# Optimization experiments

Measured on AMD Instinct MI355X. Metric: run time of the kernel, lower is better.

Reference implementation:

```python
import jax, jax.numpy as jnp
import numpy as np

EPS = 1e-6

def setup_inputs() -> dict:
    key = jax.random.key(0)
    ks = jax.random.split(key, 5)
    B, NH, S, DH = 2, 4, 2048, 128
    return {
        "q": jax.random.normal(ks[0], (B, NH, S, DH), dtype=jnp.float32),
        "k": jax.random.normal(ks[1], (B, NH, S, DH), dtype=jnp.float32),
        "v": jax.random.normal(ks[2], (B, NH, S, DH), dtype=jnp.float32),
        "i": jax.random.normal(ks[3], (B, NH, S), dtype=jnp.float32),
        "f": jax.random.normal(ks[4], (B, NH, S), dtype=jnp.float32),
    }

def _mlstm(q, k, v, i, f):
    # q,k,v: [B,NH,S,DH]; i,f: [B,NH,S] gate pre-activations.
    B, NH, S, DH = q.shape
    q = q * (DH ** -0.5)
    f_log = jax.nn.log_sigmoid(f)  # log forget gate

    # time-major for scan: [S, B, NH, ...]
    qT = jnp.moveaxis(q, 2, 0)
    kT = jnp.moveaxis(k, 2, 0)
    vT = jnp.moveaxis(v, 2, 0)
    iT = jnp.moveaxis(i, 2, 0)
    fT = jnp.moveaxis(f_log, 2, 0)

    C0 = jnp.zeros((B, NH, DH, DH), dtype=q.dtype)  # matrix memory C
    n0 = jnp.zeros((B, NH, DH), dtype=q.dtype)      # normalizer state n
    m0 = jnp.zeros((B, NH), dtype=q.dtype)          # max-stabilizer state m

    def step(carry, xs):
        C, n, m = carry
        q_t, k_t, v_t, i_t, fl_t = xs
        m_new = jnp.maximum(fl_t + m, i_t)               # [B,NH]
        a = jnp.exp(fl_t + m - m_new)                    # decay scale
        b = jnp.exp(i_t - m_new)                         # input scale
        C_new = a[..., None, None] * C + b[..., None, None] * (
            k_t[..., :, None] * v_t[..., None, :])       # [B,NH,DH,DH]
        n_new = a[..., None] * n + b[..., None] * k_t    # [B,NH,DH]
        h_num = jnp.einsum('bhd,bhde->bhe', q_t, C_new)  # [B,NH,DH]
        qn = jnp.einsum('bhd,bhd->bh', q_t, n_new)
        denom = jnp.maximum(jnp.abs(qn), jnp.exp(-m_new)) + EPS
        h = h_num / denom[..., None]
        return (C_new, n_new, m_new), h

    _, hT = jax.lax.scan(step, (C0, n0, m0), (qT, kT, vT, iT, fT))
    return jnp.moveaxis(hT, 0, 2)  # [B,NH,S,DH]

def reference(q, k, v, i, f):
    return _mlstm(q, k, v, i, f)
```

## Files before the change

kernel.cpp:

```cpp
#include <hip/hip_runtime.h>
#include <math.h>


typedef _Float16 f16;
typedef _Float16 f16x4 __attribute__((ext_vector_type(4)));
typedef _Float16 f16x8 __attribute__((ext_vector_type(8)));
typedef float    f32x4 __attribute__((ext_vector_type(4)));

#define S_LEN  2048
#define DHD    128
#define NHEADS 8
#define QT     32
#define KT     128
#define EPS    1e-6f

#define KH_OFF  0
#define KL_OFF  32768
#define VTH_OFF 65536
#define VTL_OFF 98304
#define BS_OFF  131072
#define QNL_OFF 131712
#define SMEM_BYTES 132224
#define PART_OFF 0

__device__ __forceinline__ int kswz(int row, int byteInRow) {
  return row * 256 + (byteInRow ^ ((row & 15) << 4));
}
__device__ __forceinline__ int vswz(int e, int byteInRow) {
  return e * 256 + (byteInRow ^ ((e & 15) << 4) ^ (((e >> 4) & 1) << 3));
}

__device__ __forceinline__ f32x4 mfma16(f16x8 a, f16x8 b, f32x4 c) {
  return __builtin_amdgcn_mfma_f32_16x16x32_f16(a, b, c, 0, 0, 0);
}

__global__ __launch_bounds__(256) void mlstm_scan(
    const float* __restrict__ ig_all, const float* __restrict__ fg_all,
    float* __restrict__ bf, float* __restrict__ Mf, float* __restrict__ en)
{
  const int hd  = blockIdx.x;
  const int tid = threadIdx.x;
  __shared__ double sc[256];
  const float* fg = fg_all + (size_t)hd * S_LEN;
  const float* ig = ig_all + (size_t)hd * S_LEN;
  const int base = tid * 8;

  double v[8];
#pragma unroll
  for (int u = 0; u < 8; ++u) {
    float x = fg[base + u];
    float fl = fminf(x, 0.0f) - log1pf(expf(-fabsf(x)));
    v[u] = (double)fl;
  }
#pragma unroll
  for (int u = 1; u < 8; ++u) v[u] += v[u - 1];
  sc[tid] = v[7];
  __syncthreads();
  for (int off = 1; off < 256; off <<= 1) {
    double t = (tid >= off) ? sc[tid - off] : 0.0;
    __syncthreads();
    sc[tid] += t;
    __syncthreads();
  }
  const double excl = sc[tid] - v[7];

  double F[8], b[8];
#pragma unroll
  for (int u = 0; u < 8; ++u) {
    F[u] = v[u] + excl;
    b[u] = (double)ig[base + u] - F[u];
    bf[(size_t)hd * S_LEN + base + u] = (float)b[u];
  }
  __syncthreads();
  double mv[8];
  mv[0] = b[0];
#pragma unroll
  for (int u = 1; u < 8; ++u) mv[u] = fmax(mv[u - 1], b[u]);
  sc[tid] = mv[7];
  __syncthreads();
  for (int off = 1; off < 256; off <<= 1) {
    double t = (tid >= off) ? sc[tid - off] : -1.0e300;
    __syncthreads();
    sc[tid] = fmax(sc[tid], t);
    __syncthreads();
  }
  const double exclm = (tid > 0) ? sc[tid - 1] : -1.0e300;
  double run = exclm;
#pragma unroll
  for (int u = 0; u < 8; ++u) {
    run = fmax(run, b[u]);
    double Mt = fmax(0.0, run);
    Mf[(size_t)hd * S_LEN + base + u] = (float)Mt;
    en[(size_t)hd * S_LEN + base + u] = (float)exp(-(F[u] + Mt));
  }
}

__global__ __launch_bounds__(256, 1) void mlstm_main(
    const float* __restrict__ qg, const float* __restrict__ kg, const float* __restrict__ vg,
    const float* __restrict__ bf, const float* __restrict__ Mf, const float* __restrict__ en,
    float* __restrict__ outg)
{
  extern __shared__ char smem[];
  const int bid  = blockIdx.x;
  const int hd   = bid & 7;
  const int qt32 = 63 - (bid >> 3);
  const int t0   = qt32 * QT;
  const int tid  = threadIdx.x;
  const int w    = tid >> 6;
  const int lane = tid & 63;
  const int c    = lane & 15;
  const int g    = lane >> 4;

  const size_t hbase = (size_t)hd * S_LEN;
  const float* qg_h = qg + (hbase + t0) * DHD;
  const float* kg_h = kg + hbase * DHD;
  const float* vg_h = vg + hbase * DHD;
  float* bs_lds = (float*)(smem + BS_OFF);

  constexpr float QSC = 0.08838834764831845f;
  f16x8 qfh[2][4], qfl[2][4];
#pragma unroll
  for (int qt = 0; qt < 2; ++qt) {
    const float* qrow = qg_h + (size_t)(16 * qt + c) * DHD;
#pragma unroll
    for (int kc = 0; kc < 4; ++kc) {
      const float* p = qrow + kc * 32 + 8 * g;
      float4 a = *(const float4*)p;
      float4 b = *(const float4*)(p + 4);
      float xs[8] = {a.x, a.y, a.z, a.w, b.x, b.y, b.z, b.w};
#pragma unroll
      for (int s = 0; s < 8; ++s) {
        float x = xs[s] * QSC;
        f16 hi = (f16)x;
        qfh[qt][kc][s] = hi;
        qfl[qt][kc][s] = (f16)(x - (float)hi);
      }
    }
  }

  float Mq[2];
  Mq[0] = Mf[hbase + t0 + c];
  Mq[1] = Mf[hbase + t0 + 16 + c];

  const f32x4 z4 = {0.f, 0.f, 0.f, 0.f};
  f32x4 hacc[2][8];
#pragma unroll
  for (int qt = 0; qt < 2; ++qt)
#pragma unroll
    for (int et = 0; et < 8; ++et) hacc[qt][et] = z4;
  float qn[2] = {0.f, 0.f};

  const int n_iters = qt32 / 4 + 1;
  for (int it = 0; it < n_iters; ++it) {
    const int s0 = it * KT;
    __syncthreads();

    {
      const int colq = tid & 31;
      const int r0 = tid >> 5;
#pragma unroll
      for (int pass = 0; pass < 16; ++pass) {
        const int row = pass * 8 + r0;
        float4 kv4 = *(const float4*)(kg_h + (size_t)(s0 + row) * DHD + colq * 4);
        float xs[4] = {kv4.x, kv4.y, kv4.z, kv4.w};
        f16x4 hi, lo;
#pragma unroll
        for (int s = 0; s < 4; ++s) { f16 h = (f16)xs[s]; hi[s] = h; lo[s] = (f16)(xs[s] - (float)h); }
        const int byte = kswz(row, colq * 8);
        *(f16x4*)(smem + KH_OFF + byte) = hi;
        *(f16x4*)(smem + KL_OFF + byte) = lo;
      }
      const int e   = tid & 127;
      const int kq0 = tid >> 7;
#pragma unroll
      for (int pass = 0; pass < 16; ++pass) {
        const int kvq = pass * 2 + kq0;
        const int kvb = kvq * 4;
        float xs[4];
#pragma unroll
        for (int r = 0; r < 4; ++r) xs[r] = vg_h[(size_t)(s0 + kvb + r) * DHD + e];
        f16x4 hi, lo;
#pragma unroll
        for (int s = 0; s < 4; ++s) { f16 h = (f16)xs[s]; hi[s] = h; lo[s] = (f16)(xs[s] - (float)h); }
        const int byte = vswz(e, kvq * 8);
        *(f16x4*)(smem + VTH_OFF + byte) = hi;
        *(f16x4*)(smem + VTL_OFF + byte) = lo;
      }
      if (tid < 128) bs_lds[tid] = bf[hbase + s0 + tid];
    }
    __syncthreads();

    f32x4 sacc[2][2];
    sacc[0][0] = z4; sacc[0][1] = z4; sacc[1][0] = z4; sacc[1][1] = z4;
    const int kvrow = 32 * w + c;
#pragma unroll
    for (int kc = 0; kc < 4; ++kc) {
      const int cb = kc * 64 + 16 * g;
      f16x8 kh0 = *(const f16x8*)(smem + KH_OFF + kswz(kvrow,      cb));
      f16x8 kl0 = *(const f16x8*)(smem + KL_OFF + kswz(kvrow,      cb));
      f16x8 kh1 = *(const f16x8*)(smem + KH_OFF + kswz(kvrow + 16, cb));
      f16x8 kl1 = *(const f16x8*)(smem + KL_OFF + kswz(kvrow + 16, cb));
#pragma unroll
      for (int qt = 0; qt < 2; ++qt) {
        sacc[qt][0] = mfma16(kh0, qfh[qt][kc], sacc[qt][0]);
        sacc[qt][0] = mfma16(kh0, qfl[qt][kc], sacc[qt][0]);
        sacc[qt][0] = mfma16(kl0, qfh[qt][kc], sacc[qt][0]);
        sacc[qt][1] = mfma16(kh1, qfh[qt][kc], sacc[qt][1]);
        sacc[qt][1] = mfma16(kh1, qfl[qt][kc], sacc[qt][1]);
        sacc[qt][1] = mfma16(kl1, qfh[qt][kc], sacc[qt][1]);
      }
    }

    f32x4 b0 = *(const f32x4*)(bs_lds + 32 * w + 4 * g);
    f32x4 b1 = *(const f32x4*)(bs_lds + 32 * w + 16 + 4 * g);
    f16x8 pfh[2], pfl[2];
#pragma unroll
    for (int qt = 0; qt < 2; ++qt) {
      const int qglob = t0 + 16 * qt + c;
#pragma unroll
      for (int r = 0; r < 4; ++r) {
        const int kv0 = s0 + 32 * w + 4 * g + r;
        const int kv1 = kv0 + 16;
        float p0 = (kv0 <= qglob) ? __expf(b0[r] - Mq[qt]) * sacc[qt][0][r] : 0.f;
        float p1 = (kv1 <= qglob) ? __expf(b1[r] - Mq[qt]) * sacc[qt][1][r] : 0.f;
        qn[qt] += p0 + p1;
        f16 h0 = (f16)p0; pfh[qt][r]     = h0; pfl[qt][r]     = (f16)(p0 - (float)h0);
        f16 h1 = (f16)p1; pfh[qt][r + 4] = h1; pfl[qt][r + 4] = (f16)(p1 - (float)h1);
      }
    }

#pragma unroll
    for (int et = 0; et < 8; ++et) {
      const int e = 16 * et + c;
      const int b0b = (32 * w + 4 * g) * 2;
      const int b1b = (32 * w + 16 + 4 * g) * 2;
      f16x4 vh0 = *(const f16x4*)(smem + VTH_OFF + vswz(e, b0b));
      f16x4 vh1 = *(const f16x4*)(smem + VTH_OFF + vswz(e, b1b));
      f16x4 vl0 = *(const f16x4*)(smem + VTL_OFF + vswz(e, b0b));
      f16x4 vl1 = *(const f16x4*)(smem + VTL_OFF + vswz(e, b1b));
      f16x8 vfh, vfl;
#pragma unroll
      for (int s = 0; s < 4; ++s) {
        vfh[s] = vh0[s]; vfh[s + 4] = vh1[s];
        vfl[s] = vl0[s]; vfl[s + 4] = vl1[s];
      }
#pragma unroll
      for (int qt = 0; qt < 2; ++qt) {
        hacc[qt][et] = mfma16(pfh[qt], vfh, hacc[qt][et]);
        hacc[qt][et] = mfma16(pfh[qt], vfl, hacc[qt][et]);
        hacc[qt][et] = mfma16(pfl[qt], vfh, hacc[qt][et]);
      }
    }
  }

#pragma unroll
  for (int qt = 0; qt < 2; ++qt) {
    qn[qt] += __shfl_xor(qn[qt], 16);
    qn[qt] += __shfl_xor(qn[qt], 32);
  }
  __syncthreads();
  float* qnl  = (float*)(smem + QNL_OFF);
  float* part = (float*)(smem + PART_OFF);
  if (lane < 16) { qnl[w * 32 + lane] = qn[0]; qnl[w * 32 + 16 + lane] = qn[1]; }
#pragma unroll
  for (int qt = 0; qt < 2; ++qt)
#pragma unroll
    for (int et = 0; et < 8; ++et)
#pragma unroll
      for (int r = 0; r < 4; ++r)
        part[(w * 32 + 16 * qt + 4 * g + r) * 132 + 16 * et + c] = hacc[qt][et][r];
  __syncthreads();

  const int e4 = (tid & 31) * 4;
#pragma unroll
  for (int pass = 0; pass < 4; ++pass) {
    const int q = pass * 8 + (tid >> 5);
    f32x4 s = {0.f, 0.f, 0.f, 0.f};
#pragma unroll
    for (int wv = 0; wv < 4; ++wv) {
      const float* pp = part + (wv * 32 + q) * 132 + e4;
      s[0] += pp[0]; s[1] += pp[1]; s[2] += pp[2]; s[3] += pp[3];
    }
    const float qns = qnl[q] + qnl[32 + q] + qnl[64 + q] + qnl[96 + q];
    const float den = fmaxf(fabsf(qns), en[hbase + t0 + q]) + EPS;
    const float inv = 1.0f / den;
    float4 o = make_float4(s[0] * inv, s[1] * inv, s[2] * inv, s[3] * inv);
    *(float4*)(outg + (hbase + t0 + q) * DHD + e4) = o;
  }
}

extern "C" void kernel_launch(void* const* d_in, const int* in_sizes, int n_in,
                              void* d_out, int out_size, void* d_ws, size_t ws_size,
                              hipStream_t stream) {
  (void)in_sizes; (void)n_in; (void)out_size; (void)ws_size;
  const float* q  = (const float*)d_in[0];
  const float* k  = (const float*)d_in[1];
  const float* v  = (const float*)d_in[2];
  const float* ii = (const float*)d_in[3];
  const float* ff = (const float*)d_in[4];
  float* out = (float*)d_out;

  float* bf = (float*)d_ws;
  float* Mf = bf + NHEADS * S_LEN;
  float* en = Mf + NHEADS * S_LEN;

  hipFuncSetAttribute(reinterpret_cast<const void*>(mlstm_main),
                      hipFuncAttributeMaxDynamicSharedMemorySize, SMEM_BYTES);
  mlstm_scan<<<dim3(NHEADS), dim3(256), 0, stream>>>(ii, ff, bf, Mf, en);
  mlstm_main<<<dim3(512), dim3(256), SMEM_BYTES, stream>>>(q, k, v, bf, Mf, en, out);
}
```

Before: 166.3 us.

## Precompute fp16 hi/lo K/V panels and stream them into LDS asynchronously

Adds prep kernels that split K and transposed V into swizzled fp16 hi/lo panels in workspace once per call. The main kernel then copies these panels directly into LDS with global_load_lds instead of converting them per tile. It also shrinks the KV tile to 64, splits the work across waves as 2 query halves by 2 KV halves, and halves LDS use so two blocks fit per CU. Blocks are interleaved so heavy and light causal tiles alternate. The cost is two extra launches, the extra workspace traffic, and a fallback path kept for when the workspace is too small.

```diff
diff --git a/kernel.cpp b/kernel.cpp
--- a/kernel.cpp
+++ b/kernel.cpp
@@ -10,28 +10,28 @@
 #define S_LEN  2048
 #define DHD    128
 #define NHEADS 8
-#define QT     32
-#define KT     128
 #define EPS    1e-6f
 
-#define KH_OFF  0
-#define KL_OFF  32768
-#define VTH_OFF 65536
-#define VTL_OFF 98304
-#define BS_OFF  131072
-#define QNL_OFF 131712
-#define SMEM_BYTES 132224
-#define PART_OFF 0
+#define KHI_F 0
+#define KLO_F 16384
+#define VHI_F 32768
+#define VLO_F 49152
+#define BS_F  65536
+#define QNL_F 65792
+#define SMEM_FAST 66048
 
 __device__ __forceinline__ int kswz(int row, int byteInRow) {
   return row * 256 + (byteInRow ^ ((row & 15) << 4));
 }
-__device__ __forceinline__ int vswz(int e, int byteInRow) {
-  return e * 256 + (byteInRow ^ ((e & 15) << 4) ^ (((e >> 4) & 1) << 3));
-}
-
+__device__ __forceinline__ int vswz64(int e, int byteInRow) {
+  return e * 128 + (byteInRow ^ ((e & 15) << 3));
+}
 __device__ __forceinline__ f32x4 mfma16(f16x8 a, f16x8 b, f32x4 c) {
   return __builtin_amdgcn_mfma_f32_16x16x32_f16(a, b, c, 0, 0, 0);
+}
+__device__ __forceinline__ void gload16(const void* g, void* l) {
+  __builtin_amdgcn_global_load_lds((const __attribute__((address_space(1))) unsigned int*)g,
+                                   (__attribute__((address_space(3))) unsigned int*)l, 16, 0, 0);
 }
 
 __global__ __launch_bounds__(256) void mlstm_scan(
@@ -95,7 +95,239 @@
   }
 }
 
-__global__ __launch_bounds__(256, 1) void mlstm_main(
+__global__ __launch_bounds__(256) void prep_k(
+    const float* __restrict__ kg, char* __restrict__ gkh, char* __restrict__ gkl)
+{
+  const int gid  = blockIdx.x * 256 + threadIdx.x;
+  const int row  = gid >> 2;
+  const int part = gid & 3;
+  const float* src = kg + (size_t)row * DHD;
+  char* oh = gkh + (size_t)row * 256;
+  char* ol = gkl + (size_t)row * 256;
+#pragma unroll
+  for (int j = 0; j < 8; ++j) {
+    float4 x = *(const float4*)(src + j * 16 + part * 4);
+    float xs[4] = {x.x, x.y, x.z, x.w};
+    f16x4 hi, lo;
+#pragma unroll
+    for (int s = 0; s < 4; ++s) { f16 h = (f16)xs[s]; hi[s] = h; lo[s] = (f16)(xs[s] - (float)h); }
+    const int byte = (j * 32 + part * 8) ^ ((row & 15) << 4);
+    *(f16x4*)(oh + byte) = hi;
+    *(f16x4*)(ol + byte) = lo;
+  }
+}
+
+__global__ __launch_bounds__(256) void prep_vt(
+    const float* __restrict__ vg, char* __restrict__ gvh, char* __restrict__ gvl)
+{
+  __shared__ float vts[64][132];
+  const int bid = blockIdx.x;
+  const int head = bid >> 5;
+  const int it   = bid & 31;
+  const int tid  = threadIdx.x;
+
+  {
+    const int r   = tid >> 2;
+    const int seg = tid & 3;
+    const float* src = vg + ((size_t)(head * S_LEN + it * 64 + r)) * DHD;
+#pragma unroll
+    for (int j = 0; j < 8; ++j) {
+      const int c4 = j * 16 + seg * 4;
+      *(float4*)&vts[r][c4] = *(const float4*)(src + c4);
+    }
+  }
+  __syncthreads();
+
+  const int e = tid >> 1;
+  const int h = tid & 1;
+  const size_t tb = (size_t)(head * 32 + it) * 16384 + (size_t)e * 128;
+#pragma unroll
+  for (int i4 = 0; i4 < 8; ++i4) {
+    f16x4 hi, lo;
+#pragma unroll
+    for (int s = 0; s < 4; ++s) {
+      float x = vts[32 * h + i4 * 4 + s][e];
+      f16 hh = (f16)x; hi[s] = hh; lo[s] = (f16)(x - (float)hh);
+    }
+    const int byte = ((32 * h + i4 * 4) * 2) ^ ((e & 15) << 3);
+    *(f16x4*)(gvh + tb + byte) = hi;
+    *(f16x4*)(gvl + tb + byte) = lo;
+  }
+}
+
+__global__ __launch_bounds__(256, 2) void mlstm_fast(
+    const float* __restrict__ qg,
+    const char* __restrict__ gkh, const char* __restrict__ gkl,
+    const char* __restrict__ gvh, const char* __restrict__ gvl,
+    const float* __restrict__ bf, const float* __restrict__ Mf,
+    const float* __restrict__ en, float* __restrict__ outg)
+{
+  extern __shared__ char smem[];
+  const int bid  = blockIdx.x;
+  const int hd   = bid & 7;
+  const int idx  = bid >> 3;
+  const int qt32 = (idx < 32) ? (63 - 2 * idx) : (2 * (idx - 32));
+  const int t0   = qt32 * 32;
+  const int tid  = threadIdx.x;
+  const int w    = tid >> 6;
+  const int lane = tid & 63;
+  const int c    = lane & 15;
+  const int g    = lane >> 4;
+  const int wk   = w & 1;
+  const int qh   = w >> 1;
+
+  const size_t hbase = (size_t)hd * S_LEN;
+  float* bs_lds = (float*)(smem + BS_F);
+
+  constexpr float QSC = 0.08838834764831845f;
+  f16x8 qfh[4], qfl[4];
+  {
+    const float* qrow = qg + (hbase + t0 + 16 * qh + c) * DHD;
+#pragma unroll
+    for (int kc = 0; kc < 4; ++kc) {
+      const float* p = qrow + kc * 32 + 8 * g;
+      float4 a = *(const float4*)p;
+      float4 b = *(const float4*)(p + 4);
+      float xs[8] = {a.x, a.y, a.z, a.w, b.x, b.y, b.z, b.w};
+#pragma unroll
+      for (int s = 0; s < 8; ++s) {
+        float x = xs[s] * QSC;
+        f16 hi = (f16)x;
+        qfh[kc][s] = hi;
+        qfl[kc][s] = (f16)(x - (float)hi);
+      }
+    }
+  }
+  const float Mq = Mf[hbase + t0 + 16 * qh + c];
+
+  const f32x4 z4 = {0.f, 0.f, 0.f, 0.f};
+  f32x4 hacc[8];
+#pragma unroll
+  for (int et = 0; et < 8; ++et) hacc[et] = z4;
+  float qn = 0.f;
+
+  const char* pkh = gkh + hbase * 256;
+  const char* pkl = gkl + hbase * 256;
+  const char* pvh = gvh + (size_t)hd * 524288;
+  const char* pvl = gvl + (size_t)hd * 524288;
+
+  const int n_iters = qt32 / 2 + 1;
+  for (int it = 0; it < n_iters; ++it) {
+    const int s0 = it * 64;
+    __syncthreads();
+
+    {
+      const size_t tb = (size_t)it * 16384;
+#pragma unroll
+      for (int u = 0; u < 4; ++u) {
+        const int off = (w << 12) + (u << 10);
+        const int gl  = off + lane * 16;
+        gload16(pkh + tb + gl, smem + KHI_F + off);
+        gload16(pkl + tb + gl, smem + KLO_F + off);
+        gload16(pvh + tb + gl, smem + VHI_F + off);
+        gload16(pvl + tb + gl, smem + VLO_F + off);
+      }
+      if (tid < 64) bs_lds[tid] = bf[hbase + s0 + tid];
+    }
+    __syncthreads();
+
+    f32x4 sacc0 = z4, sacc1 = z4;
+    const int rowA = 32 * wk + c;
+#pragma unroll
+    for (int kc = 0; kc < 4; ++kc) {
+      const int cb = kc * 64 + 16 * g;
+      f16x8 kh0 = *(const f16x8*)(smem + KHI_F + kswz(rowA,      cb));
+      f16x8 kl0 = *(const f16x8*)(smem + KLO_F + kswz(rowA,      cb));
+      f16x8 kh1 = *(const f16x8*)(smem + KHI_F + kswz(rowA + 16, cb));
+      f16x8 kl1 = *(const f16x8*)(smem + KLO_F + kswz(rowA + 16, cb));
+      sacc0 = mfma16(kh0, qfh[kc], sacc0);
+      sacc0 = mfma16(kh0, qfl[kc], sacc0);
+      sacc0 = mfma16(kl0, qfh[kc], sacc0);
+      sacc1 = mfma16(kh1, qfh[kc], sacc1);
+      sacc1 = mfma16(kh1, qfl[kc], sacc1);
+      sacc1 = mfma16(kl1, qfh[kc], sacc1);
+    }
+
+    f32x4 b0 = *(const f32x4*)(bs_lds + 32 * wk + 4 * g);
+    f32x4 b1 = *(const f32x4*)(bs_lds + 32 * wk + 16 + 4 * g);
+    const int qglob = t0 + 16 * qh + c;
+    f16x8 pfh, pfl;
+#pragma unroll
+    for (int r = 0; r < 4; ++r) {
+      const int kv0 = s0 + 32 * wk + 4 * g + r;
+      const int kv1 = kv0 + 16;
+      float p0 = (kv0 <= qglob) ? __expf(b0[r] - Mq) * sacc0[r] : 0.f;
+      float p1 = (kv1 <= qglob) ? __expf(b1[r] - Mq) * sacc1[r] : 0.f;
+      qn += p0 + p1;
+      f16 h0 = (f16)p0; pfh[r]     = h0; pfl[r]     = (f16)(p0 - (float)h0);
+      f16 h1 = (f16)p1; pfh[r + 4] = h1; pfl[r + 4] = (f16)(p1 - (float)h1);
+    }
+
+    const int byte0 = (64 * wk + 8 * g)      ^ (c << 3);
+    const int byte1 = (64 * wk + 32 + 8 * g) ^ (c << 3);
+#pragma unroll
+    for (int et = 0; et < 8; ++et) {
+      const int eb = (16 * et + c) * 128;
+      f16x4 vh0 = *(const f16x4*)(smem + VHI_F + eb + byte0);
+      f16x4 vh1 = *(const f16x4*)(smem + VHI_F + eb + byte1);
+      f16x4 vl0 = *(const f16x4*)(smem + VLO_F + eb + byte0);
+      f16x4 vl1 = *(const f16x4*)(smem + VLO_F + eb + byte1);
+      f16x8 vfh, vfl;
+#pragma unroll
+      for (int s = 0; s < 4; ++s) {
+        vfh[s] = vh0[s]; vfh[s + 4] = vh1[s];
+        vfl[s] = vl0[s]; vfl[s + 4] = vl1[s];
+      }
+      hacc[et] = mfma16(pfh, vfh, hacc[et]);
+      hacc[et] = mfma16(pfh, vfl, hacc[et]);
+      hacc[et] = mfma16(pfl, vfh, hacc[et]);
+    }
+  }
+
+  qn += __shfl_xor(qn, 16);
+  qn += __shfl_xor(qn, 32);
+  __syncthreads();
+  float* qnl  = (float*)(smem + QNL_F);
+  float* part = (float*)smem;
+  if (lane < 16) qnl[(wk * 2 + qh) * 16 + lane] = qn;
+#pragma unroll
+  for (int et = 0; et < 8; ++et)
+#pragma unroll
+    for (int r = 0; r < 4; ++r)
+      part[(wk * 32 + 16 * qh + 4 * g + r) * 132 + 16 * et + c] = hacc[et][r];
+  __syncthreads();
+
+  const int e4 = (tid & 31) * 4;
+#pragma unroll
+  for (int pass = 0; pass < 4; ++pass) {
+    const int q = pass * 8 + (tid >> 5);
+    const float* pa = part + q * 132 + e4;
+    const float* pb = part + (32 + q) * 132 + e4;
+    f32x4 s;
+#pragma unroll
+    for (int s_ = 0; s_ < 4; ++s_) s[s_] = pa[s_] + pb[s_];
+    const int qhh = q >> 4;
+    const float qns = qnl[qhh * 16 + (q & 15)] + qnl[(2 + qhh) * 16 + (q & 15)];
+    const float den = fmaxf(fabsf(qns), en[hbase + t0 + q]) + EPS;
+    const float inv = 1.0f / den;
+    float4 o = make_float4(s[0] * inv, s[1] * inv, s[2] * inv, s[3] * inv);
+    *(float4*)(outg + (hbase + t0 + q) * DHD + e4) = o;
+  }
+}
+
+#define KH_OFF  0
+#define KL_OFF  32768
+#define VTH_OFF 65536
+#define VTL_OFF 98304
+#define BS_OFF  131072
+#define QNL_OFF 131712
+#define SMEM_FB 132224
+
+__device__ __forceinline__ int vswzfb(int e, int byteInRow) {
+  return e * 256 + (byteInRow ^ ((e & 15) << 4) ^ (((e >> 4) & 1) << 3));
+}
+
+__global__ __launch_bounds__(256, 1) void mlstm_main_fb(
     const float* __restrict__ qg, const float* __restrict__ kg, const float* __restrict__ vg,
     const float* __restrict__ bf, const float* __restrict__ Mf, const float* __restrict__ en,
     float* __restrict__ outg)
@@ -104,7 +336,7 @@
   const int bid  = blockIdx.x;
   const int hd   = bid & 7;
   const int qt32 = 63 - (bid >> 3);
-  const int t0   = qt32 * QT;
+  const int t0   = qt32 * 32;
   const int tid  = threadIdx.x;
   const int w    = tid >> 6;
   const int lane = tid & 63;
@@ -137,7 +369,6 @@
       }
     }
   }
-
   float Mq[2];
   Mq[0] = Mf[hbase + t0 + c];
   Mq[1] = Mf[hbase + t0 + 16 + c];
@@ -152,9 +383,8 @@
 
   const int n_iters = qt32 / 4 + 1;
   for (int it = 0; it < n_iters; ++it) {
-    const int s0 = it * KT;
-    __syncthreads();
-
+    const int s0 = it * 128;
+    __syncthreads();
     {
       const int colq = tid & 31;
       const int r0 = tid >> 5;
@@ -182,7 +412,7 @@
         f16x4 hi, lo;
 #pragma unroll
         for (int s = 0; s < 4; ++s) { f16 h = (f16)xs[s]; hi[s] = h; lo[s] = (f16)(xs[s] - (float)h); }
-        const int byte = vswz(e, kvq * 8);
+        const int byte = vswzfb(e, kvq * 8);
         *(f16x4*)(smem + VTH_OFF + byte) = hi;
         *(f16x4*)(smem + VTL_OFF + byte) = lo;
       }
@@ -234,10 +464,10 @@
       const int e = 16 * et + c;
       const int b0b = (32 * w + 4 * g) * 2;
       const int b1b = (32 * w + 16 + 4 * g) * 2;
-      f16x4 vh0 = *(const f16x4*)(smem + VTH_OFF + vswz(e, b0b));
-      f16x4 vh1 = *(const f16x4*)(smem + VTH_OFF + vswz(e, b1b));
-      f16x4 vl0 = *(const f16x4*)(smem + VTL_OFF + vswz(e, b0b));
-      f16x4 vl1 = *(const f16x4*)(smem + VTL_OFF + vswz(e, b1b));
+      f16x4 vh0 = *(const f16x4*)(smem + VTH_OFF + vswzfb(e, b0b));
+      f16x4 vh1 = *(const f16x4*)(smem + VTH_OFF + vswzfb(e, b1b));
+      f16x4 vl0 = *(const f16x4*)(smem + VTL_OFF + vswzfb(e, b0b));
+      f16x4 vl1 = *(const f16x4*)(smem + VTL_OFF + vswzfb(e, b1b));
       f16x8 vfh, vfl;
 #pragma unroll
       for (int s = 0; s < 4; ++s) {
@@ -260,7 +490,7 @@
   }
   __syncthreads();
   float* qnl  = (float*)(smem + QNL_OFF);
-  float* part = (float*)(smem + PART_OFF);
+  float* part = (float*)smem;
   if (lane < 16) { qnl[w * 32 + lane] = qn[0]; qnl[w * 32 + 16 + lane] = qn[1]; }
 #pragma unroll
   for (int qt = 0; qt < 2; ++qt)
@@ -292,7 +522,7 @@
 extern "C" void kernel_launch(void* const* d_in, const int* in_sizes, int n_in,
                               void* d_out, int out_size, void* d_ws, size_t ws_size,
                               hipStream_t stream) {
-  (void)in_sizes; (void)n_in; (void)out_size; (void)ws_size;
+  (void)in_sizes; (void)n_in; (void)out_size;
   const float* q  = (const float*)d_in[0];
   const float* k  = (const float*)d_in[1];
   const float* v  = (const float*)d_in[2];
@@ -304,8 +534,26 @@
   float* Mf = bf + NHEADS * S_LEN;
   float* en = Mf + NHEADS * S_LEN;
 
-  hipFuncSetAttribute(reinterpret_cast<const void*>(mlstm_main),
-                      hipFuncAttributeMaxDynamicSharedMemorySize, SMEM_BYTES);
+  const size_t PANEL = 4u * 1024 * 1024;
+  const size_t need  = 3u * NHEADS * S_LEN * 4 + 4 * PANEL;
+
   mlstm_scan<<<dim3(NHEADS), dim3(256), 0, stream>>>(ii, ff, bf, Mf, en);
-  mlstm_main<<<dim3(512), dim3(256), SMEM_BYTES, stream>>>(q, k, v, bf, Mf, en, out);
-}
+
+  if (ws_size >= need) {
+    char* gkh = (char*)(en + NHEADS * S_LEN);
+    char* gkl = gkh + PANEL;
+    char* gvh = gkl + PANEL;
+    char* gvl = gvh + PANEL;
+    hipFuncSetAttribute(reinterpret_cast<const void*>(mlstm_fast),
+                        hipFuncAttributeMaxDynamicSharedMemorySize, SMEM_FAST);
+    prep_k <<<dim3(256), dim3(256), 0, stream>>>(k, gkh, gkl);
+    prep_vt<<<dim3(256), dim3(256), 0, stream>>>(v, gvh, gvl);
+    mlstm_fast<<<dim3(512), dim3(256), SMEM_FAST, stream>>>(
+        q, gkh, gkl, gvh, gvl, bf, Mf, en, out);
+  } else {
+    hipFuncSetAttribute(reinterpret_cast<const void*>(mlstm_main_fb),
+                        hipFuncAttributeMaxDynamicSharedMemorySize, SMEM_FB);
+    mlstm_main_fb<<<dim3(512), dim3(256), SMEM_FB, stream>>>(
+        q, k, v, bf, Mf, en, out);
+  }
+}
```

Result: faster. 159.8 us (-3.9%).

## Precompute fp16 hi/lo K/V panels and double-buffer async LDS loads

Applied to the files above, without the earlier changes.

A new prep kernel converts K and V once into swizzled fp16 hi/lo panels in workspace, with V transposed per 64-row tile. The main kernel then streams those panels into LDS with global_load_lds into a double buffer, prefetching the next tile while computing the current one. It also uses 64-query blocks with 64-key tiles split across wave pairs, halving the grid. The aim is to remove the repeated per-block fp32-to-fp16 split and V transpose and to overlap loads with MFMA work. The cost is an extra kernel launch, extra workspace traffic, and fewer blocks, with a heavier causal load imbalance that is no longer reversed-order scheduled.

```diff
diff --git a/kernel.cpp b/kernel.cpp
--- a/kernel.cpp
+++ b/kernel.cpp
@@ -10,28 +10,21 @@
 #define S_LEN  2048
 #define DHD    128
 #define NHEADS 8
-#define QT     32
-#define KT     128
 #define EPS    1e-6f
 
-#define KH_OFF  0
-#define KL_OFF  32768
-#define VTH_OFF 65536
-#define VTL_OFF 98304
-#define BS_OFF  131072
-#define QNL_OFF 131712
-#define SMEM_BYTES 132224
-#define PART_OFF 0
+#define BUFSZ   65536
+#define QNL_OFF 131072
+#define SMEM_BYTES 131584
 
 __device__ __forceinline__ int kswz(int row, int byteInRow) {
   return row * 256 + (byteInRow ^ ((row & 15) << 4));
 }
-__device__ __forceinline__ int vswz(int e, int byteInRow) {
-  return e * 256 + (byteInRow ^ ((e & 15) << 4) ^ (((e >> 4) & 1) << 3));
-}
-
 __device__ __forceinline__ f32x4 mfma16(f16x8 a, f16x8 b, f32x4 c) {
   return __builtin_amdgcn_mfma_f32_16x16x32_f16(a, b, c, 0, 0, 0);
+}
+__device__ __forceinline__ void gload16(const void* g, void* l) {
+  __builtin_amdgcn_global_load_lds((const __attribute__((address_space(1))) unsigned int*)g,
+                                   (__attribute__((address_space(3))) unsigned int*)l, 16, 0, 0);
 }
 
 __global__ __launch_bounds__(256) void mlstm_scan(
@@ -95,33 +88,112 @@
   }
 }
 
-__global__ __launch_bounds__(256, 1) void mlstm_main(
-    const float* __restrict__ qg, const float* __restrict__ kg, const float* __restrict__ vg,
-    const float* __restrict__ bf, const float* __restrict__ Mf, const float* __restrict__ en,
-    float* __restrict__ outg)
+__global__ __launch_bounds__(256) void mlstm_prep(
+    const float* __restrict__ kg, const float* __restrict__ vg,
+    char* __restrict__ gkh, char* __restrict__ gkl,
+    char* __restrict__ gvh, char* __restrict__ gvl)
+{
+  __shared__ float vts[64][132];
+  const int bid = blockIdx.x;
+  const int tid = threadIdx.x;
+
+  if (bid < 256) {
+    const int gid  = bid * 256 + tid;
+    const int row  = gid >> 2;
+    const int part = gid & 3;
+    const float* src = kg + (size_t)row * DHD;
+    char* oh = gkh + (size_t)row * 256;
+    char* ol = gkl + (size_t)row * 256;
+#pragma unroll
+    for (int j = 0; j < 8; ++j) {
+      float4 x = *(const float4*)(src + j * 16 + part * 4);
+      float xs[4] = {x.x, x.y, x.z, x.w};
+      f16x4 hi, lo;
+#pragma unroll
+      for (int s = 0; s < 4; ++s) { f16 h = (f16)xs[s]; hi[s] = h; lo[s] = (f16)(xs[s] - (float)h); }
+      const int byte = (j * 32 + part * 8) ^ ((row & 15) << 4);
+      *(f16x4*)(oh + byte) = hi;
+      *(f16x4*)(ol + byte) = lo;
+    }
+  } else {
+    const int b2   = bid - 256;
+    const int head = b2 >> 5;
+    const int it   = b2 & 31;
+    {
+      const int r   = tid >> 2;
+      const int seg = tid & 3;
+      const float* src = vg + ((size_t)(head * S_LEN + it * 64 + r)) * DHD;
+#pragma unroll
+      for (int j = 0; j < 8; ++j) {
+        const int c4 = j * 16 + seg * 4;
+        *(float4*)&vts[r][c4] = *(const float4*)(src + c4);
+      }
+    }
+    __syncthreads();
+    const int e = tid >> 1;
+    const int h = tid & 1;
+    const size_t tb = (size_t)(head * 32 + it) * 16384 + (size_t)e * 128;
+#pragma unroll
+    for (int i4 = 0; i4 < 8; ++i4) {
+      f16x4 hi, lo;
+#pragma unroll
+      for (int s = 0; s < 4; ++s) {
+        float x = vts[32 * h + i4 * 4 + s][e];
+        f16 hh = (f16)x; hi[s] = hh; lo[s] = (f16)(x - (float)hh);
+      }
+      const int byte = ((32 * h + i4 * 4) * 2) ^ ((e & 15) << 3);
+      *(f16x4*)(gvh + tb + byte) = hi;
+      *(f16x4*)(gvl + tb + byte) = lo;
+    }
+  }
+}
+
+__global__ __launch_bounds__(256, 1) void mlstm_fast2(
+    const float* __restrict__ qg,
+    const char* __restrict__ gkh, const char* __restrict__ gkl,
+    const char* __restrict__ gvh, const char* __restrict__ gvl,
+    const float* __restrict__ bf, const float* __restrict__ Mf,
+    const float* __restrict__ en, float* __restrict__ outg)
 {
   extern __shared__ char smem[];
   const int bid  = blockIdx.x;
   const int hd   = bid & 7;
-  const int qt32 = 63 - (bid >> 3);
-  const int t0   = qt32 * QT;
+  const int j    = bid >> 3;
+  const int t0   = j * 64;
   const int tid  = threadIdx.x;
   const int w    = tid >> 6;
   const int lane = tid & 63;
   const int c    = lane & 15;
   const int g    = lane >> 4;
+  const int wk   = w & 1;
+  const int qp   = w >> 1;
 
   const size_t hbase = (size_t)hd * S_LEN;
-  const float* qg_h = qg + (hbase + t0) * DHD;
-  const float* kg_h = kg + hbase * DHD;
-  const float* vg_h = vg + hbase * DHD;
-  float* bs_lds = (float*)(smem + BS_OFF);
+  const char* pkh = gkh + hbase * 256;
+  const char* pkl = gkl + hbase * 256;
+  const char* pvh = gvh + (size_t)hd * 524288;
+  const char* pvl = gvl + (size_t)hd * 524288;
+
+  const int n_it = j + 1;
+
+  {
+    const size_t tb = 0;
+#pragma unroll
+    for (int u = 0; u < 4; ++u) {
+      const int off = (w << 12) + (u << 10);
+      const int gl  = off + lane * 16;
+      gload16(pkh + tb + gl, smem + 0     + off);
+      gload16(pkl + tb + gl, smem + 16384 + off);
+      gload16(pvh + tb + gl, smem + 32768 + off);
+      gload16(pvl + tb + gl, smem + 49152 + off);
+    }
+  }
 
   constexpr float QSC = 0.08838834764831845f;
   f16x8 qfh[2][4], qfl[2][4];
 #pragma unroll
-  for (int qt = 0; qt < 2; ++qt) {
-    const float* qrow = qg_h + (size_t)(16 * qt + c) * DHD;
+  for (int u = 0; u < 2; ++u) {
+    const float* qrow = qg + (hbase + t0 + 16 * (2 * qp + u) + c) * DHD;
 #pragma unroll
     for (int kc = 0; kc < 4; ++kc) {
       const float* p = qrow + kc * 32 + 8 * g;
@@ -132,112 +204,92 @@
       for (int s = 0; s < 8; ++s) {
         float x = xs[s] * QSC;
         f16 hi = (f16)x;
-        qfh[qt][kc][s] = hi;
-        qfl[qt][kc][s] = (f16)(x - (float)hi);
-      }
-    }
-  }
-
+        qfh[u][kc][s] = hi;
+        qfl[u][kc][s] = (f16)(x - (float)hi);
+      }
+    }
+  }
   float Mq[2];
-  Mq[0] = Mf[hbase + t0 + c];
-  Mq[1] = Mf[hbase + t0 + 16 + c];
+  Mq[0] = Mf[hbase + t0 + 16 * (2 * qp) + c];
+  Mq[1] = Mf[hbase + t0 + 16 * (2 * qp + 1) + c];
 
   const f32x4 z4 = {0.f, 0.f, 0.f, 0.f};
   f32x4 hacc[2][8];
 #pragma unroll
-  for (int qt = 0; qt < 2; ++qt)
-#pragma unroll
-    for (int et = 0; et < 8; ++et) hacc[qt][et] = z4;
+  for (int u = 0; u < 2; ++u)
+#pragma unroll
+    for (int et = 0; et < 8; ++et) hacc[u][et] = z4;
   float qn[2] = {0.f, 0.f};
 
-  const int n_iters = qt32 / 4 + 1;
-  for (int it = 0; it < n_iters; ++it) {
-    const int s0 = it * KT;
-    __syncthreads();
-
-    {
-      const int colq = tid & 31;
-      const int r0 = tid >> 5;
-#pragma unroll
-      for (int pass = 0; pass < 16; ++pass) {
-        const int row = pass * 8 + r0;
-        float4 kv4 = *(const float4*)(kg_h + (size_t)(s0 + row) * DHD + colq * 4);
-        float xs[4] = {kv4.x, kv4.y, kv4.z, kv4.w};
-        f16x4 hi, lo;
-#pragma unroll
-        for (int s = 0; s < 4; ++s) { f16 h = (f16)xs[s]; hi[s] = h; lo[s] = (f16)(xs[s] - (float)h); }
-        const int byte = kswz(row, colq * 8);
-        *(f16x4*)(smem + KH_OFF + byte) = hi;
-        *(f16x4*)(smem + KL_OFF + byte) = lo;
-      }
-      const int e   = tid & 127;
-      const int kq0 = tid >> 7;
-#pragma unroll
-      for (int pass = 0; pass < 16; ++pass) {
-        const int kvq = pass * 2 + kq0;
-        const int kvb = kvq * 4;
-        float xs[4];
-#pragma unroll
-        for (int r = 0; r < 4; ++r) xs[r] = vg_h[(size_t)(s0 + kvb + r) * DHD + e];
-        f16x4 hi, lo;
-#pragma unroll
-        for (int s = 0; s < 4; ++s) { f16 h = (f16)xs[s]; hi[s] = h; lo[s] = (f16)(xs[s] - (float)h); }
-        const int byte = vswz(e, kvq * 8);
-        *(f16x4*)(smem + VTH_OFF + byte) = hi;
-        *(f16x4*)(smem + VTL_OFF + byte) = lo;
-      }
-      if (tid < 128) bs_lds[tid] = bf[hbase + s0 + tid];
-    }
-    __syncthreads();
+  int cur = 0;
+  for (int it = 0; it < n_it; ++it) {
+    const int s0 = it * 64;
+    __syncthreads();
+
+    f32x4 b0 = *(const f32x4*)(bf + hbase + s0 + 32 * wk + 4 * g);
+    f32x4 b1 = *(const f32x4*)(bf + hbase + s0 + 32 * wk + 16 + 4 * g);
+
+    if (it + 1 < n_it) {
+      const size_t tb = (size_t)(it + 1) * 16384;
+      char* lb = smem + (cur ^ 1) * BUFSZ;
+#pragma unroll
+      for (int u = 0; u < 4; ++u) {
+        const int off = (w << 12) + (u << 10);
+        const int gl  = off + lane * 16;
+        gload16(pkh + tb + gl, lb + 0     + off);
+        gload16(pkl + tb + gl, lb + 16384 + off);
+        gload16(pvh + tb + gl, lb + 32768 + off);
+        gload16(pvl + tb + gl, lb + 49152 + off);
+      }
+    }
+
+    const char* lb = smem + cur * BUFSZ;
 
     f32x4 sacc[2][2];
     sacc[0][0] = z4; sacc[0][1] = z4; sacc[1][0] = z4; sacc[1][1] = z4;
-    const int kvrow = 32 * w + c;
 #pragma unroll
     for (int kc = 0; kc < 4; ++kc) {
       const int cb = kc * 64 + 16 * g;
-      f16x8 kh0 = *(const f16x8*)(smem + KH_OFF + kswz(kvrow,      cb));
-      f16x8 kl0 = *(const f16x8*)(smem + KL_OFF + kswz(kvrow,      cb));
-      f16x8 kh1 = *(const f16x8*)(smem + KH_OFF + kswz(kvrow + 16, cb));
-      f16x8 kl1 = *(const f16x8*)(smem + KL_OFF + kswz(kvrow + 16, cb));
-#pragma unroll
-      for (int qt = 0; qt < 2; ++qt) {
-        sacc[qt][0] = mfma16(kh0, qfh[qt][kc], sacc[qt][0]);
-        sacc[qt][0] = mfma16(kh0, qfl[qt][kc], sacc[qt][0]);
-        sacc[qt][0] = mfma16(kl0, qfh[qt][kc], sacc[qt][0]);
-        sacc[qt][1] = mfma16(kh1, qfh[qt][kc], sacc[qt][1]);
-        sacc[qt][1] = mfma16(kh1, qfl[qt][kc], sacc[qt][1]);
-        sacc[qt][1] = mfma16(kl1, qfh[qt][kc], sacc[qt][1]);
-      }
-    }
-
-    f32x4 b0 = *(const f32x4*)(bs_lds + 32 * w + 4 * g);
-    f32x4 b1 = *(const f32x4*)(bs_lds + 32 * w + 16 + 4 * g);
+      f16x8 kh0 = *(const f16x8*)(lb + 0     + kswz(32 * wk + c,      cb));
+      f16x8 kl0 = *(const f16x8*)(lb + 16384 + kswz(32 * wk + c,      cb));
+      f16x8 kh1 = *(const f16x8*)(lb + 0     + kswz(32 * wk + 16 + c, cb));
+      f16x8 kl1 = *(const f16x8*)(lb + 16384 + kswz(32 * wk + 16 + c, cb));
+#pragma unroll
+      for (int u = 0; u < 2; ++u) {
+        sacc[u][0] = mfma16(kh0, qfh[u][kc], sacc[u][0]);
+        sacc[u][0] = mfma16(kh0, qfl[u][kc], sacc[u][0]);
+        sacc[u][0] = mfma16(kl0, qfh[u][kc], sacc[u][0]);
+        sacc[u][1] = mfma16(kh1, qfh[u][kc], sacc[u][1]);
+        sacc[u][1] = mfma16(kh1, qfl[u][kc], sacc[u][1]);
+        sacc[u][1] = mfma16(kl1, qfh[u][kc], sacc[u][1]);
+      }
+    }
+
     f16x8 pfh[2], pfl[2];
 #pragma unroll
-    for (int qt = 0; qt < 2; ++qt) {
-      const int qglob = t0 + 16 * qt + c;
+    for (int u = 0; u < 2; ++u) {
+      const int qglob = t0 + 16 * (2 * qp + u) + c;
 #pragma unroll
       for (int r = 0; r < 4; ++r) {
-        const int kv0 = s0 + 32 * w + 4 * g + r;
+        const int kv0 = s0 + 32 * wk + 4 * g + r;
         const int kv1 = kv0 + 16;
-        float p0 = (kv0 <= qglob) ? __expf(b0[r] - Mq[qt]) * sacc[qt][0][r] : 0.f;
-        float p1 = (kv1 <= qglob) ? __expf(b1[r] - Mq[qt]) * sacc[qt][1][r] : 0.f;
-        qn[qt] += p0 + p1;
-        f16 h0 = (f16)p0; pfh[qt][r]     = h0; pfl[qt][r]     = (f16)(p0 - (float)h0);
-        f16 h1 = (f16)p1; pfh[qt][r + 4] = h1; pfl[qt][r + 4] = (f16)(p1 - (float)h1);
-      }
-    }
-
+        float p0 = (kv0 <= qglob) ? __expf(b0[r] - Mq[u]) * sacc[u][0][r] : 0.f;
+        float p1 = (kv1 <= qglob) ? __expf(b1[r] - Mq[u]) * sacc[u][1][r] : 0.f;
+        qn[u] += p0 + p1;
+        f16 h0 = (f16)p0; pfh[u][r]     = h0; pfl[u][r]     = (f16)(p0 - (float)h0);
+        f16 h1 = (f16)p1; pfh[u][r + 4] = h1; pfl[u][r + 4] = (f16)(p1 - (float)h1);
+      }
+    }
+
+    const int byte0 = (64 * wk + 8 * g)      ^ (c << 3);
+    const int byte1 = (64 * wk + 32 + 8 * g) ^ (c << 3);
 #pragma unroll
     for (int et = 0; et < 8; ++et) {
-      const int e = 16 * et + c;
-      const int b0b = (32 * w + 4 * g) * 2;
-      const int b1b = (32 * w + 16 + 4 * g) * 2;
-      f16x4 vh0 = *(const f16x4*)(smem + VTH_OFF + vswz(e, b0b));
-      f16x4 vh1 = *(const f16x4*)(smem + VTH_OFF + vswz(e, b1b));
-      f16x4 vl0 = *(const f16x4*)(smem + VTL_OFF + vswz(e, b0b));
-      f16x4 vl1 = *(const f16x4*)(smem + VTL_OFF + vswz(e, b1b));
+      const int eb = (16 * et + c) * 128;
+      f16x4 vh0 = *(const f16x4*)(lb + 32768 + eb + byte0);
+      f16x4 vh1 = *(const f16x4*)(lb + 32768 + eb + byte1);
+      f16x4 vl0 = *(const f16x4*)(lb + 49152 + eb + byte0);
+      f16x4 vl1 = *(const f16x4*)(lb + 49152 + eb + byte1);
       f16x8 vfh, vfl;
 #pragma unroll
       for (int s = 0; s < 4; ++s) {
@@ -245,43 +297,46 @@
         vfl[s] = vl0[s]; vfl[s + 4] = vl1[s];
       }
 #pragma unroll
-      for (int qt = 0; qt < 2; ++qt) {
-        hacc[qt][et] = mfma16(pfh[qt], vfh, hacc[qt][et]);
-        hacc[qt][et] = mfma16(pfh[qt], vfl, hacc[qt][et]);
-        hacc[qt][et] = mfma16(pfl[qt], vfh, hacc[qt][et]);
-      }
-    }
-  }
-
-#pragma unroll
-  for (int qt = 0; qt < 2; ++qt) {
-    qn[qt] += __shfl_xor(qn[qt], 16);
-    qn[qt] += __shfl_xor(qn[qt], 32);
+      for (int u = 0; u < 2; ++u) {
+        hacc[u][et] = mfma16(pfh[u], vfh, hacc[u][et]);
+        hacc[u][et] = mfma16(pfh[u], vfl, hacc[u][et]);
+        hacc[u][et] = mfma16(pfl[u], vfh, hacc[u][et]);
+      }
+    }
+    cur ^= 1;
+  }
+
+#pragma unroll
+  for (int u = 0; u < 2; ++u) {
+    qn[u] += __shfl_xor(qn[u], 16);
+    qn[u] += __shfl_xor(qn[u], 32);
   }
   __syncthreads();
   float* qnl  = (float*)(smem + QNL_OFF);
-  float* part = (float*)(smem + PART_OFF);
-  if (lane < 16) { qnl[w * 32 + lane] = qn[0]; qnl[w * 32 + 16 + lane] = qn[1]; }
-#pragma unroll
-  for (int qt = 0; qt < 2; ++qt)
+  float* part = (float*)smem;
+  if (lane < 16) {
+    qnl[(wk * 4 + 2 * qp + 0) * 16 + lane] = qn[0];
+    qnl[(wk * 4 + 2 * qp + 1) * 16 + lane] = qn[1];
+  }
+#pragma unroll
+  for (int u = 0; u < 2; ++u)
 #pragma unroll
     for (int et = 0; et < 8; ++et)
 #pragma unroll
       for (int r = 0; r < 4; ++r)
-        part[(w * 32 + 16 * qt + 4 * g + r) * 132 + 16 * et + c] = hacc[qt][et][r];
+        part[(wk * 64 + 16 * (2 * qp + u) + 4 * g + r) * 132 + 16 * et + c] = hacc[u][et][r];
   __syncthreads();
 
   const int e4 = (tid & 31) * 4;
 #pragma unroll
-  for (int pass = 0; pass < 4; ++pass) {
+  for (int pass = 0; pass < 8; ++pass) {
     const int q = pass * 8 + (tid >> 5);
-    f32x4 s = {0.f, 0.f, 0.f, 0.f};
-#pragma unroll
-    for (int wv = 0; wv < 4; ++wv) {
-      const float* pp = part + (wv * 32 + q) * 132 + e4;
-      s[0] += pp[0]; s[1] += pp[1]; s[2] += pp[2]; s[3] += pp[3];
-    }
-    const float qns = qnl[q] + qnl[32 + q] + qnl[64 + q] + qnl[96 + q];
+    const float* pa = part + q * 132 + e4;
+    const float* pb = part + (64 + q) * 132 + e4;
+    f32x4 s;
+#pragma unroll
+    for (int s_ = 0; s_ < 4; ++s_) s[s_] = pa[s_] + pb[s_];
+    const float qns = qnl[(q >> 4) * 16 + (q & 15)] + qnl[(4 + (q >> 4)) * 16 + (q & 15)];
     const float den = fmaxf(fabsf(qns), en[hbase + t0 + q]) + EPS;
     const float inv = 1.0f / den;
     float4 o = make_float4(s[0] * inv, s[1] * inv, s[2] * inv, s[3] * inv);
@@ -304,8 +359,16 @@
   float* Mf = bf + NHEADS * S_LEN;
   float* en = Mf + NHEADS * S_LEN;
 
-  hipFuncSetAttribute(reinterpret_cast<const void*>(mlstm_main),
+  const size_t PANEL = 4u * 1024 * 1024;
+  char* gkh = (char*)(en + NHEADS * S_LEN);
+  char* gkl = gkh + PANEL;
+  char* gvh = gkl + PANEL;
+  char* gvl = gvh + PANEL;
+
+  hipFuncSetAttribute(reinterpret_cast<const void*>(mlstm_fast2),
                       hipFuncAttributeMaxDynamicSharedMemorySize, SMEM_BYTES);
   mlstm_scan<<<dim3(NHEADS), dim3(256), 0, stream>>>(ii, ff, bf, Mf, en);
-  mlstm_main<<<dim3(512), dim3(256), SMEM_BYTES, stream>>>(q, k, v, bf, Mf, en, out);
-}
+  mlstm_prep<<<dim3(512), dim3(256), 0, stream>>>(k, v, gkh, gkl, gvh, gvl);
+  mlstm_fast2<<<dim3(256), dim3(256), SMEM_BYTES, stream>>>(
+      q, gkh, gkl, gvh, gvl, bf, Mf, en, out);
+}
```

Result: no change. 164.0 us (-1.4%).
